# Kernel tuning notes

Hardware: AMD Instinct MI355X
Metric: run time of the kernel (lower is better)

## Reference

```python
import jax, jax.numpy as jnp
import numpy as np

EPS = 1e-5
C = 128
N, H, W = 16, 128, 128


def bn(x, g, b, m, v):
    # x: (N, C, H, W) or (N, C); params: (C,)
    sh = (1, -1) + (1,) * (x.ndim - 2)
    return (x - m.reshape(sh)) * (g.reshape(sh) / jnp.sqrt(v.reshape(sh) + EPS)) + b.reshape(sh)


def conv1x1(x, w, b=None):
    # x: (N, Cin, H, W), w: (Cout, Cin)
    y = jnp.einsum('oc,nchw->nohw', w, x)
    if b is not None:
        y = y + b.reshape(1, -1, 1, 1)
    return y


def setup_inputs() -> dict:
    key = jax.random.key(0)
    ks = jax.random.split(key, 20)
    C2 = C // 2
    Cr = C // 16
    d = {
        'f_vi': jax.random.normal(ks[0], (N, C, H, W), jnp.float32),
        'f_ir': jax.random.normal(ks[1], (N, C, H, W), jnp.float32),
        # channel_avg_attention: conv(2C->C/2)+BN+ReLU+conv(C/2->C)+BN+Sigmoid
        'ca1_w': jax.random.normal(ks[2], (C2, 2 * C), jnp.float32) * 0.05,
        'ca1_b': jnp.zeros((C2,), jnp.float32),
        'bn_a_g': jnp.ones((C2,), jnp.float32),
        'bn_a_b': jnp.zeros((C2,), jnp.float32),
        'bn_a_m': jnp.zeros((C2,), jnp.float32),
        'bn_a_v': jnp.ones((C2,), jnp.float32),
        'ca2_w': jax.random.normal(ks[3], (C, C2), jnp.float32) * 0.05,
        'ca2_b': jnp.zeros((C,), jnp.float32),
        'bn_b_g': jnp.ones((C,), jnp.float32),
        'bn_b_b': jnp.zeros((C,), jnp.float32),
        'bn_b_m': jnp.zeros((C,), jnp.float32),
        'bn_b_v': jnp.ones((C,), jnp.float32),
        # conv1: conv(2C->C)+BN+ReLU
        'conv1_w': jax.random.normal(ks[4], (C, 2 * C), jnp.float32) * 0.05,
        'conv1_b': jnp.zeros((C,), jnp.float32),
        'bn_c_g': jnp.ones((C,), jnp.float32),
        'bn_c_b': jnp.zeros((C,), jnp.float32),
        'bn_c_m': jnp.zeros((C,), jnp.float32),
        'bn_c_v': jnp.ones((C,), jnp.float32),
        # ChannelAttention shared MLP (no bias)
        'chatt_w1': jax.random.normal(ks[5], (Cr, C), jnp.float32) * 0.1,
        'chatt_w2': jax.random.normal(ks[6], (C, Cr), jnp.float32) * 0.1,
        # SpatialAttention 7x7 conv (no bias), (out=1, in=2, 7, 7)
        'sa_w': jax.random.normal(ks[7], (1, 2, 7, 7), jnp.float32) * 0.05,
    }
    return d


def reference(f_vi, f_ir, ca1_w, ca1_b, bn_a_g, bn_a_b, bn_a_m, bn_a_v,
              ca2_w, ca2_b, bn_b_g, bn_b_b, bn_b_m, bn_b_v,
              conv1_w, conv1_b, bn_c_g, bn_c_b, bn_c_m, bn_c_v,
              chatt_w1, chatt_w2, sa_w):
    c = f_vi.shape[1]
    f_cat = jnp.concatenate([f_vi, f_ir], axis=1)  # (N, 2C, H, W)

    # channel_avg_attention: GAP -> 1x1 conv -> BN -> ReLU -> 1x1 conv -> BN -> Sigmoid
    pooled = jnp.mean(f_cat, axis=(2, 3))  # (N, 2C)
    h = jax.nn.relu(bn(pooled @ ca1_w.T + ca1_b, bn_a_g, bn_a_b, bn_a_m, bn_a_v))
    wch = jax.nn.sigmoid(bn(h @ ca2_w.T + ca2_b, bn_b_g, bn_b_b, bn_b_m, bn_b_v))  # (N, C)
    w2 = jnp.concatenate([wch, wch], axis=1)[:, :, None, None]  # (N, 2C, 1, 1)

    f_cat = jnp.concatenate([f_ir, f_vi], axis=1) * w2 + f_cat  # complementary blend
    f_vi2, f_ir2 = f_cat[:, :c], f_cat[:, c:]

    g = jax.nn.relu(bn(conv1x1(f_cat, conv1_w, conv1_b), bn_c_g, bn_c_b, bn_c_m, bn_c_v))  # (N, C, H, W)

    # ChannelAttention on g
    avg = jnp.mean(g, axis=(2, 3))  # (N, C)
    mx = jnp.max(g, axis=(2, 3))    # (N, C)
    mlp = lambda x: jax.nn.relu(x @ chatt_w1.T) @ chatt_w2.T
    ca = jax.nn.sigmoid(mlp(avg) + mlp(mx))[:, :, None, None]  # (N, C, 1, 1)

    # SpatialAttention on g
    sp = jnp.stack([jnp.mean(g, axis=1), jnp.max(g, axis=1)], axis=1)  # (N, 2, H, W)
    sa = jax.lax.conv_general_dilated(sp, sa_w, window_strides=(1, 1), padding=[(3, 3), (3, 3)],
                                      dimension_numbers=('NCHW', 'OIHW', 'NCHW'))
    sa = jax.nn.sigmoid(sa)  # (N, 1, H, W)

    wgt = jax.nn.sigmoid(sa * ca)  # (N, C, H, W)
    return wgt * f_vi2 + (1.0 - wgt) * f_ir2
```

## Files before the change

### kernel.cpp

```cpp
#include <hip/hip_runtime.h>
#include <math.h>

#define CCH   128
#define C2    64
#define C2X   256
#define CR    8
#define HW    16384
#define NB    16
#define EPSB  1e-5f

#define WS_POOLED 0
#define WS_WCH    4096
#define WS_AVGS   6144
#define WS_MAXB   8192
#define WS_CA     10240
#define WS_BC     12288
#define WS_WV     16384
#define WS_WI     147456
#define WS_SPMEAN 278528
#define WS_SPMAX  540672
#define WS_SA     802816

typedef short short8 __attribute__((ext_vector_type(8)));
typedef float floatx4 __attribute__((ext_vector_type(4)));
typedef unsigned short ushort_t;
typedef unsigned int uint_t;

__device__ __forceinline__ float sigmoidf_(float x) {
    return 1.0f / (1.0f + __expf(-x));
}

__device__ __forceinline__ uint_t f2bf(float f) {
    uint_t u = __float_as_uint(f);
    return (u + 0x7FFFu + ((u >> 16) & 1u)) >> 16;
}
__device__ __forceinline__ uint_t pack2bf(float a, float b) {
    return f2bf(a) | (f2bf(b) << 16);
}

__global__ void k_pool(const float* __restrict__ fvi, const float* __restrict__ fir,
                       float* __restrict__ pooled) {
    int b  = blockIdx.x;
    int n  = b >> 8;
    int ch = b & 255;
    const float* src = (ch < CCH) ? (fvi + ((size_t)n * CCH + ch) * HW)
                                  : (fir + ((size_t)n * CCH + (ch - CCH)) * HW);
    const float4* s4 = (const float4*)src;
    float s0 = 0.f, s1 = 0.f, s2 = 0.f, s3 = 0.f;
    #pragma unroll
    for (int it = 0; it < 4; ++it) {
        float4 v0 = s4[threadIdx.x + (it * 4 + 0) * 256];
        float4 v1 = s4[threadIdx.x + (it * 4 + 1) * 256];
        float4 v2 = s4[threadIdx.x + (it * 4 + 2) * 256];
        float4 v3 = s4[threadIdx.x + (it * 4 + 3) * 256];
        s0 += (v0.x + v0.y) + (v0.z + v0.w);
        s1 += (v1.x + v1.y) + (v1.z + v1.w);
        s2 += (v2.x + v2.y) + (v2.z + v2.w);
        s3 += (v3.x + v3.y) + (v3.z + v3.w);
    }
    float sum = (s0 + s1) + (s2 + s3);
    #pragma unroll
    for (int off = 32; off > 0; off >>= 1) sum += __shfl_down(sum, off, 64);
    __shared__ float r[4];
    if ((threadIdx.x & 63) == 0) r[threadIdx.x >> 6] = sum;
    __syncthreads();
    if (threadIdx.x == 0)
        pooled[b] = (r[0] + r[1] + r[2] + r[3]) * (1.0f / HW);
}

__global__ void k_wch(const float* __restrict__ pooled,
                      const float* __restrict__ ca1_w, const float* __restrict__ ca1_b,
                      const float* __restrict__ ag, const float* __restrict__ ab,
                      const float* __restrict__ am, const float* __restrict__ av,
                      const float* __restrict__ ca2_w, const float* __restrict__ ca2_b,
                      const float* __restrict__ bg, const float* __restrict__ bb,
                      const float* __restrict__ bm, const float* __restrict__ bv,
                      float* __restrict__ wch) {
    int n = blockIdx.x;
    int t = threadIdx.x;
    __shared__ float h[C2];
    if (t < C2) {
        float acc = ca1_b[t];
        const float* w = ca1_w + t * C2X;
        const float* p = pooled + n * C2X;
        for (int k = 0; k < C2X; k++) acc += w[k] * p[k];
        float s = ag[t] * rsqrtf(av[t] + EPSB);
        acc = (acc - am[t]) * s + ab[t];
        h[t] = fmaxf(acc, 0.f);
    }
    __syncthreads();
    float acc = ca2_b[t];
    const float* w = ca2_w + t * C2;
    for (int j = 0; j < C2; j++) acc += w[j] * h[j];
    float s = bg[t] * rsqrtf(bv[t] + EPSB);
    acc = (acc - bm[t]) * s + bb[t];
    wch[n * CCH + t] = sigmoidf_(acc);
}

__global__ void k_mkweights(const float* __restrict__ wch, const float* __restrict__ conv1_w,
                            const float* __restrict__ cg, const float* __restrict__ cb,
                            const float* __restrict__ cm, const float* __restrict__ cv,
                            const float* __restrict__ conv1_b,
                            ushort_t* __restrict__ Wv, ushort_t* __restrict__ Wi,
                            float* __restrict__ Bc, float* __restrict__ zeroreg) {
    int b = blockIdx.x;
    int t = threadIdx.x;
    if (b < 16) { zeroreg[b * 256 + t] = 0.f; zeroreg[b * 256 + 128 + t] = 0.f; }
    if (b == 16) {
        float A = cg[t] * rsqrtf(cv[t] + EPSB);
        Bc[t] = A * (conv1_b[t] - cm[t]) + cb[t];
    }
    int n = b >> 7, o = b & 127;
    float A  = cg[o] * rsqrtf(cv[o] + EPSB);
    float u  = wch[n * CCH + t];
    float w0 = conv1_w[o * C2X + t];
    float w1 = conv1_w[o * C2X + t + CCH];
    Wv[(size_t)b * CCH + t] = (ushort_t)f2bf(A * (w0 + u * w1));
    Wi[(size_t)b * CCH + t] = (ushort_t)f2bf(A * (w1 + u * w0));
}

#define XR 64
__global__ __launch_bounds__(256)
void k_conv_reduce(const float* __restrict__ fvi, const float* __restrict__ fir,
                   const ushort_t* __restrict__ Wv, const ushort_t* __restrict__ Wi,
                   const float* __restrict__ Bc,
                   float* __restrict__ avgsum, uint_t* __restrict__ maxbits,
                   float* __restrict__ spmean, float* __restrict__ spmax) {
    int n  = blockIdx.x >> 7;
    int pt = blockIdx.x & 127;
    int p0 = pt * 128;

    __shared__ __align__(16) ushort_t sW[128 * XR];
    __shared__ __align__(16) ushort_t sX[128 * XR];

    int tid  = threadIdx.x;
    int wave = tid >> 6;
    int lane = tid & 63;
    int q    = lane >> 4;
    int ln   = lane & 15;

    floatx4 acc[2][8];
    #pragma unroll
    for (int a = 0; a < 2; a++)
        #pragma unroll
        for (int b = 0; b < 8; b++) acc[a][b] = (floatx4){0.f, 0.f, 0.f, 0.f};

    const float* pv = fvi + (size_t)n * CCH * HW + p0;
    const float* pi = fir + (size_t)n * CCH * HW + p0;
    const ushort_t* wvb = Wv + (size_t)n * CCH * CCH;
    const ushort_t* wib = Wi + (size_t)n * CCH * CCH;

    int wo  = tid >> 2, wc = tid & 3;
    int xpq = tid & 15, xcp = tid >> 4;
    int xch = xcp >> 2, xdw = xcp & 3;

    for (int ks = 0; ks < 8; ++ks) {
        const ushort_t* wsrc = (ks < 4) ? wvb : wib;
        const float*    xsrc = (ks < 4) ? pv  : pi;
        int c0 = (ks & 3) * 32;

        __syncthreads();
        #pragma unroll
        for (int it = 0; it < 2; ++it) {
            int o = it * 64 + wo;
            uint4 w4 = *(const uint4*)&wsrc[(size_t)o * CCH + c0 + wc * 8];
            *(uint4*)&sW[o * XR + ((wc ^ (o & 7)) << 3)] = w4;
        }
        #pragma unroll
        for (int it = 0; it < 2; ++it) {
            int pq = (it << 4) | xpq;
            const float* sp = xsrc + (size_t)(c0 + 2 * xcp) * HW + 4 * pq;
            float4 f1 = *(const float4*)sp;
            float4 f2 = *(const float4*)(sp + HW);
            int r0 = 4 * pq;
            *(uint_t*)&sX[(r0 + 0) * XR + ((xch ^ ((r0 + 0) & 7)) << 3) + xdw * 2] = pack2bf(f1.x, f2.x);
            *(uint_t*)&sX[(r0 + 1) * XR + ((xch ^ ((r0 + 1) & 7)) << 3) + xdw * 2] = pack2bf(f1.y, f2.y);
            *(uint_t*)&sX[(r0 + 2) * XR + ((xch ^ ((r0 + 2) & 7)) << 3) + xdw * 2] = pack2bf(f1.z, f2.z);
            *(uint_t*)&sX[(r0 + 3) * XR + ((xch ^ ((r0 + 3) & 7)) << 3) + xdw * 2] = pack2bf(f1.w, f2.w);
        }
        __syncthreads();

        short8 aW0, aW1;
        {
            int rA0 = wave * 32 + ln;
            int rA1 = rA0 + 16;
            aW0 = *(const short8*)&sW[rA0 * XR + ((q ^ (rA0 & 7)) << 3)];
            aW1 = *(const short8*)&sW[rA1 * XR + ((q ^ (rA1 & 7)) << 3)];
        }
        #pragma unroll
        for (int pj = 0; pj < 8; ++pj) {
            int rB = pj * 16 + ln;
            short8 bX = *(const short8*)&sX[rB * XR + ((q ^ (rB & 7)) << 3)];
            acc[0][pj] = __builtin_amdgcn_mfma_f32_16x16x32_bf16(aW0, bX, acc[0][pj], 0, 0, 0);
            acc[1][pj] = __builtin_amdgcn_mfma_f32_16x16x32_bf16(aW1, bX, acc[1][pj], 0, 0, 0);
        }
    }

    float bc[2][4];
    #pragma unroll
    for (int ot = 0; ot < 2; ++ot)
        #pragma unroll
        for (int r = 0; r < 4; ++r)
            bc[ot][r] = Bc[wave * 32 + ot * 16 + q * 4 + r];

    float rs[2][4], rm[2][4], ps[8], pm[8];
    #pragma unroll
    for (int ot = 0; ot < 2; ++ot)
        #pragma unroll
        for (int r = 0; r < 4; ++r) { rs[ot][r] = 0.f; rm[ot][r] = 0.f; }
    #pragma unroll
    for (int pj = 0; pj < 8; ++pj) { ps[pj] = 0.f; pm[pj] = 0.f; }

    #pragma unroll
    for (int ot = 0; ot < 2; ++ot)
        #pragma unroll
        for (int pj = 0; pj < 8; ++pj) {
            floatx4 a = acc[ot][pj];
            #pragma unroll
            for (int r = 0; r < 4; ++r) {
                float g = fmaxf(a[r] + bc[ot][r], 0.f);
                rs[ot][r] += g;
                rm[ot][r] = fmaxf(rm[ot][r], g);
                ps[pj] += g;
                pm[pj] = fmaxf(pm[pj], g);
            }
        }

    #pragma unroll
    for (int ot = 0; ot < 2; ++ot)
        #pragma unroll
        for (int r = 0; r < 4; ++r)
            #pragma unroll
            for (int off = 1; off < 16; off <<= 1) {
                rs[ot][r] += __shfl_xor(rs[ot][r], off, 64);
                rm[ot][r] = fmaxf(rm[ot][r], __shfl_xor(rm[ot][r], off, 64));
            }
    if (ln == 0) {
        #pragma unroll
        for (int ot = 0; ot < 2; ++ot)
            #pragma unroll
            for (int r = 0; r < 4; ++r) {
                int o = wave * 32 + ot * 16 + q * 4 + r;
                atomicAdd(&avgsum[n * CCH + o], rs[ot][r]);
                atomicMax(&maxbits[n * CCH + o], __float_as_uint(rm[ot][r]));
            }
    }

    #pragma unroll
    for (int pj = 0; pj < 8; ++pj) {
        #pragma unroll
        for (int off = 16; off < 64; off <<= 1) {
            ps[pj] += __shfl_xor(ps[pj], off, 64);
            pm[pj] = fmaxf(pm[pj], __shfl_xor(pm[pj], off, 64));
        }
    }
    __syncthreads();
    float* redS = (float*)sW;
    float* redM = (float*)sX;
    if (lane < 16) {
        #pragma unroll
        for (int pj = 0; pj < 8; ++pj) {
            redS[wave * 128 + pj * 16 + ln] = ps[pj];
            redM[wave * 128 + pj * 16 + ln] = pm[pj];
        }
    }
    __syncthreads();
    if (tid < 128) {
        float s = 0.f, m = 0.f;
        #pragma unroll
        for (int w = 0; w < 4; ++w) {
            s += redS[w * 128 + tid];
            m = fmaxf(m, redM[w * 128 + tid]);
        }
        spmean[(size_t)n * HW + p0 + tid] = s * (1.0f / CCH);
        spmax [(size_t)n * HW + p0 + tid] = m;
    }
}

__global__ void k_ca(const float* __restrict__ avgsum, const uint_t* __restrict__ maxbits,
                     const float* __restrict__ w1, const float* __restrict__ w2,
                     float* __restrict__ ca) {
    int n = blockIdx.x;
    int t = threadIdx.x;
    __shared__ float tsum[CR];
    if (t < CR) {
        float a = 0.f, m = 0.f;
        const float* w = w1 + t * CCH;
        for (int c = 0; c < CCH; c++) {
            a += w[c] * (avgsum[n * CCH + c] * (1.0f / HW));
            m += w[c] * __uint_as_float(maxbits[n * CCH + c]);
        }
        tsum[t] = fmaxf(a, 0.f) + fmaxf(m, 0.f);
    }
    __syncthreads();
    float s = 0.f;
    #pragma unroll
    for (int j = 0; j < CR; j++) s += w2[t * CR + j] * tsum[j];
    ca[n * CCH + t] = sigmoidf_(s);
}

__global__ void k_sa(const float* __restrict__ spmean, const float* __restrict__ spmax,
                     const float* __restrict__ sw, float* __restrict__ sa) {
    int b = blockIdx.x;
    int n = b >> 6;
    int y = ((b & 63) << 1) | (threadIdx.x >> 7);
    int x = threadIdx.x & 127;
    float acc = 0.f;
    for (int dy = -3; dy <= 3; dy++) {
        int yy = y + dy;
        if ((unsigned)yy >= 128u) continue;
        const float* rm = spmean + (size_t)n * HW + yy * 128;
        const float* rx = spmax  + (size_t)n * HW + yy * 128;
        #pragma unroll
        for (int dx = -3; dx <= 3; dx++) {
            int xx = x + dx;
            if ((unsigned)xx < 128u) {
                float wm = sw[(dy + 3) * 7 + (dx + 3)];
                float wx = sw[49 + (dy + 3) * 7 + (dx + 3)];
                acc += wm * rm[xx] + wx * rx[xx];
            }
        }
    }
    sa[(size_t)n * HW + y * 128 + x] = sigmoidf_(acc);
}

__global__ void k_out(const float4* __restrict__ fvi, const float4* __restrict__ fir,
                      const float* __restrict__ wch, const float* __restrict__ ca,
                      const float4* __restrict__ sa, float4* __restrict__ out) {
    size_t i0 = ((size_t)blockIdx.x * 256 + threadIdx.x) * 2;
    size_t i1 = i0 + 1;
    float4 a0 = fvi[i0], a1 = fvi[i1];
    float4 b0 = fir[i0], b1 = fir[i1];
    int p40 = (int)(i0 & 4095);
    int nc  = (int)(i0 >> 12);
    int n   = nc >> 7;
    float4 s0 = sa[(size_t)n * 4096 + p40];
    float4 s1 = sa[(size_t)n * 4096 + p40 + 1];
    float u  = wch[nc];
    float cv = ca[nc];
    float4 o0, o1;
    {
        float w = sigmoidf_(s0.x * cv);
        o0.x = w * (b0.x * u + a0.x) + (1.f - w) * (a0.x * u + b0.x);
    }
    {
        float w = sigmoidf_(s0.y * cv);
        o0.y = w * (b0.y * u + a0.y) + (1.f - w) * (a0.y * u + b0.y);
    }
    {
        float w = sigmoidf_(s0.z * cv);
        o0.z = w * (b0.z * u + a0.z) + (1.f - w) * (a0.z * u + b0.z);
    }
    {
        float w = sigmoidf_(s0.w * cv);
        o0.w = w * (b0.w * u + a0.w) + (1.f - w) * (a0.w * u + b0.w);
    }
    {
        float w = sigmoidf_(s1.x * cv);
        o1.x = w * (b1.x * u + a1.x) + (1.f - w) * (a1.x * u + b1.x);
    }
    {
        float w = sigmoidf_(s1.y * cv);
        o1.y = w * (b1.y * u + a1.y) + (1.f - w) * (a1.y * u + b1.y);
    }
    {
        float w = sigmoidf_(s1.z * cv);
        o1.z = w * (b1.z * u + a1.z) + (1.f - w) * (a1.z * u + b1.z);
    }
    {
        float w = sigmoidf_(s1.w * cv);
        o1.w = w * (b1.w * u + a1.w) + (1.f - w) * (a1.w * u + b1.w);
    }
    out[i0] = o0;
    out[i1] = o1;
}

extern "C" void kernel_launch(void* const* d_in, const int* in_sizes, int n_in,
                              void* d_out, int out_size, void* d_ws, size_t ws_size,
                              hipStream_t stream) {
    const float* fvi     = (const float*)d_in[0];
    const float* fir     = (const float*)d_in[1];
    const float* ca1_w   = (const float*)d_in[2];
    const float* ca1_b   = (const float*)d_in[3];
    const float* bn_a_g  = (const float*)d_in[4];
    const float* bn_a_b  = (const float*)d_in[5];
    const float* bn_a_m  = (const float*)d_in[6];
    const float* bn_a_v  = (const float*)d_in[7];
    const float* ca2_w   = (const float*)d_in[8];
    const float* ca2_b   = (const float*)d_in[9];
    const float* bn_b_g  = (const float*)d_in[10];
    const float* bn_b_b  = (const float*)d_in[11];
    const float* bn_b_m  = (const float*)d_in[12];
    const float* bn_b_v  = (const float*)d_in[13];
    const float* conv1_w = (const float*)d_in[14];
    const float* conv1_b = (const float*)d_in[15];
    const float* bn_c_g  = (const float*)d_in[16];
    const float* bn_c_b  = (const float*)d_in[17];
    const float* bn_c_m  = (const float*)d_in[18];
    const float* bn_c_v  = (const float*)d_in[19];
    const float* chatt_w1 = (const float*)d_in[20];
    const float* chatt_w2 = (const float*)d_in[21];
    const float* sa_w     = (const float*)d_in[22];

    float* ws = (float*)d_ws;
    float* out = (float*)d_out;

    k_pool<<<NB * C2X, 256, 0, stream>>>(fvi, fir, ws + WS_POOLED);
    k_wch<<<NB, 128, 0, stream>>>(ws + WS_POOLED, ca1_w, ca1_b,
                                  bn_a_g, bn_a_b, bn_a_m, bn_a_v,
                                  ca2_w, ca2_b, bn_b_g, bn_b_b, bn_b_m, bn_b_v,
                                  ws + WS_WCH);
    k_mkweights<<<NB * CCH, 128, 0, stream>>>(ws + WS_WCH, conv1_w,
                                              bn_c_g, bn_c_b, bn_c_m, bn_c_v, conv1_b,
                                              (ushort_t*)(ws + WS_WV), (ushort_t*)(ws + WS_WI),
                                              ws + WS_BC, ws + WS_AVGS);
    k_conv_reduce<<<NB * (HW / 128), 256, 0, stream>>>(fvi, fir,
                                                       (const ushort_t*)(ws + WS_WV),
                                                       (const ushort_t*)(ws + WS_WI),
                                                       ws + WS_BC,
                                                       ws + WS_AVGS, (uint_t*)(ws + WS_MAXB),
                                                       ws + WS_SPMEAN, ws + WS_SPMAX);
    k_ca<<<NB, 128, 0, stream>>>(ws + WS_AVGS, (const uint_t*)(ws + WS_MAXB),
                                 chatt_w1, chatt_w2, ws + WS_CA);
    k_sa<<<NB * 64, 256, 0, stream>>>(ws + WS_SPMEAN, ws + WS_SPMAX, sa_w, ws + WS_SA);
    k_out<<<(NB * CCH * HW / 4) / 512, 256, 0, stream>>>((const float4*)fvi, (const float4*)fir,
                                                         ws + WS_WCH, ws + WS_CA,
                                                         (const float4*)(ws + WS_SA), (float4*)out);
}
```

Before: 538.2 us.

## Fuse pooling with bf16 pre-packing and stream packed tiles into conv via LDS loads

The pooling kernel now also converts fvi/fir into swizzled bf16 tiles, written to the output buffer as scratch, and accumulates channel means with atomics after a separate zeroing kernel. The conv kernel keeps all weight fragments in registers and loads the packed tiles straight into LDS with global_load_lds, overlapping the second half of the load with MFMAs on the first. This replaces the fp32 re-read and per-iteration conversion and sync inside the conv with half-size bf16 reads. In exchange it adds an extra write and read of the bf16 blob, many atomics, and large LDS and register use. The output kernel's indexing is also changed to a coalesced stride.

```diff
diff --git a/kernel.cpp b/kernel.cpp
--- a/kernel.cpp
+++ b/kernel.cpp
@@ -26,6 +26,13 @@
 typedef unsigned short ushort_t;
 typedef unsigned int uint_t;
 
+#define GAS __attribute__((address_space(1)))
+#define LAS __attribute__((address_space(3)))
+
+__device__ __forceinline__ void gload16(const void* g, void* l) {
+    __builtin_amdgcn_global_load_lds((const GAS void*)g, (LAS void*)l, 16, 0, 0);
+}
+
 __device__ __forceinline__ float sigmoidf_(float x) {
     return 1.0f / (1.0f + __expf(-x));
 }
@@ -38,34 +45,53 @@
     return f2bf(a) | (f2bf(b) << 16);
 }
 
-__global__ void k_pool(const float* __restrict__ fvi, const float* __restrict__ fir,
-                       float* __restrict__ pooled) {
+__global__ void k_zero(float* __restrict__ p) {
+    p[blockIdx.x * 256 + threadIdx.x] = 0.f;
+}
+
+__global__ __launch_bounds__(256)
+void k_prep(const float* __restrict__ fvi, const float* __restrict__ fir,
+            ushort_t* __restrict__ blob, float* __restrict__ pooled) {
     int b  = blockIdx.x;
+    int st = b & 1;
+    int pt = (b >> 1) & 127;
     int n  = b >> 8;
-    int ch = b & 255;
-    const float* src = (ch < CCH) ? (fvi + ((size_t)n * CCH + ch) * HW)
-                                  : (fir + ((size_t)n * CCH + (ch - CCH)) * HW);
-    const float4* s4 = (const float4*)src;
-    float s0 = 0.f, s1 = 0.f, s2 = 0.f, s3 = 0.f;
-    #pragma unroll
-    for (int it = 0; it < 4; ++it) {
-        float4 v0 = s4[threadIdx.x + (it * 4 + 0) * 256];
-        float4 v1 = s4[threadIdx.x + (it * 4 + 1) * 256];
-        float4 v2 = s4[threadIdx.x + (it * 4 + 2) * 256];
-        float4 v3 = s4[threadIdx.x + (it * 4 + 3) * 256];
-        s0 += (v0.x + v0.y) + (v0.z + v0.w);
-        s1 += (v1.x + v1.y) + (v1.z + v1.w);
-        s2 += (v2.x + v2.y) + (v2.z + v2.w);
-        s3 += (v3.x + v3.y) + (v3.z + v3.w);
-    }
-    float sum = (s0 + s1) + (s2 + s3);
-    #pragma unroll
-    for (int off = 32; off > 0; off >>= 1) sum += __shfl_down(sum, off, 64);
-    __shared__ float r[4];
-    if ((threadIdx.x & 63) == 0) r[threadIdx.x >> 6] = sum;
+    const float* src = (st == 0 ? fvi : fir) + (size_t)n * CCH * HW + pt * 128;
+    __shared__ __align__(16) ushort_t img[128 * 128];
+    int t = threadIdx.x;
+    int p = t & 127;
+    int cg = t >> 7;
+    const float inv = 1.0f / HW;
+    #pragma unroll
+    for (int i = 0; i < 8; ++i) {
+        int cidx = cg * 8 + i;
+        const float* sc = src + (size_t)(cidx * 8) * HW + p;
+        float v0 = sc[0];        float v1 = sc[HW];
+        float v2 = sc[2 * HW];   float v3 = sc[3 * HW];
+        float v4 = sc[4 * HW];   float v5 = sc[5 * HW];
+        float v6 = sc[6 * HW];   float v7 = sc[7 * HW];
+        uint4 pk;
+        pk.x = pack2bf(v0, v1);  pk.y = pack2bf(v2, v3);
+        pk.z = pack2bf(v4, v5);  pk.w = pack2bf(v6, v7);
+        *(uint4*)&img[p * 128 + ((cidx ^ (p & 7)) << 3)] = pk;
+        float ss[8] = {v0, v1, v2, v3, v4, v5, v6, v7};
+        #pragma unroll
+        for (int j = 0; j < 8; ++j) {
+            float s = ss[j] * inv;
+            #pragma unroll
+            for (int off = 1; off < 64; off <<= 1)
+                s += __shfl_xor(s, off, 64);
+            if ((t & 63) == 0)
+                atomicAdd(&pooled[n * 256 + st * 128 + cidx * 8 + j], s);
+        }
+    }
     __syncthreads();
-    if (threadIdx.x == 0)
-        pooled[b] = (r[0] + r[1] + r[2] + r[3]) * (1.0f / HW);
+    ushort_t* dst = blob + (size_t)b * 16384;
+    #pragma unroll
+    for (int j = 0; j < 8; ++j) {
+        int off = (j * 256 + t) * 8;
+        *(uint4*)&dst[off] = *(const uint4*)&img[off];
+    }
 }
 
 __global__ void k_wch(const float* __restrict__ pooled,
@@ -119,9 +145,8 @@
     Wi[(size_t)b * CCH + t] = (ushort_t)f2bf(A * (w1 + u * w0));
 }
 
-#define XR 64
 __global__ __launch_bounds__(256)
-void k_conv_reduce(const float* __restrict__ fvi, const float* __restrict__ fir,
+void k_conv_reduce(const ushort_t* __restrict__ blob,
                    const ushort_t* __restrict__ Wv, const ushort_t* __restrict__ Wi,
                    const float* __restrict__ Bc,
                    float* __restrict__ avgsum, uint_t* __restrict__ maxbits,
@@ -129,70 +154,69 @@
     int n  = blockIdx.x >> 7;
     int pt = blockIdx.x & 127;
     int p0 = pt * 128;
-
-    __shared__ __align__(16) ushort_t sW[128 * XR];
-    __shared__ __align__(16) ushort_t sX[128 * XR];
-
+    __shared__ __align__(16) ushort_t sX[32768];
     int tid  = threadIdx.x;
     int wave = tid >> 6;
     int lane = tid & 63;
     int q    = lane >> 4;
     int ln   = lane & 15;
 
+    short8 aF[2][8];
+    {
+        const ushort_t* wv = Wv + (size_t)n * 16384;
+        const ushort_t* wi = Wi + (size_t)n * 16384;
+        #pragma unroll
+        for (int kc = 0; kc < 8; ++kc) {
+            const ushort_t* ws_ = (kc < 4) ? wv : wi;
+            #pragma unroll
+            for (int ot = 0; ot < 2; ++ot) {
+                int o = wave * 32 + ot * 16 + ln;
+                aF[ot][kc] = *(const short8*)&ws_[(size_t)o * 128 + (kc & 3) * 32 + q * 8];
+            }
+        }
+    }
+    __builtin_amdgcn_sched_barrier(0);
+    {
+        const ushort_t* gb = blob + (((size_t)(n * 128 + pt)) << 15) + wave * 512 + lane * 8;
+        ushort_t* lb = &sX[wave * 512];
+        #pragma unroll
+        for (int i = 0; i < 16; ++i)
+            gload16(gb + i * 2048, lb + i * 2048);
+    }
+    __builtin_amdgcn_sched_barrier(0);
+
     floatx4 acc[2][8];
     #pragma unroll
     for (int a = 0; a < 2; a++)
         #pragma unroll
-        for (int b = 0; b < 8; b++) acc[a][b] = (floatx4){0.f, 0.f, 0.f, 0.f};
-
-    const float* pv = fvi + (size_t)n * CCH * HW + p0;
-    const float* pi = fir + (size_t)n * CCH * HW + p0;
-    const ushort_t* wvb = Wv + (size_t)n * CCH * CCH;
-    const ushort_t* wib = Wi + (size_t)n * CCH * CCH;
-
-    int wo  = tid >> 2, wc = tid & 3;
-    int xpq = tid & 15, xcp = tid >> 4;
-    int xch = xcp >> 2, xdw = xcp & 3;
-
-    for (int ks = 0; ks < 8; ++ks) {
-        const ushort_t* wsrc = (ks < 4) ? wvb : wib;
-        const float*    xsrc = (ks < 4) ? pv  : pi;
-        int c0 = (ks & 3) * 32;
-
-        __syncthreads();
-        #pragma unroll
-        for (int it = 0; it < 2; ++it) {
-            int o = it * 64 + wo;
-            uint4 w4 = *(const uint4*)&wsrc[(size_t)o * CCH + c0 + wc * 8];
-            *(uint4*)&sW[o * XR + ((wc ^ (o & 7)) << 3)] = w4;
-        }
-        #pragma unroll
-        for (int it = 0; it < 2; ++it) {
-            int pq = (it << 4) | xpq;
-            const float* sp = xsrc + (size_t)(c0 + 2 * xcp) * HW + 4 * pq;
-            float4 f1 = *(const float4*)sp;
-            float4 f2 = *(const float4*)(sp + HW);
-            int r0 = 4 * pq;
-            *(uint_t*)&sX[(r0 + 0) * XR + ((xch ^ ((r0 + 0) & 7)) << 3) + xdw * 2] = pack2bf(f1.x, f2.x);
-            *(uint_t*)&sX[(r0 + 1) * XR + ((xch ^ ((r0 + 1) & 7)) << 3) + xdw * 2] = pack2bf(f1.y, f2.y);
-            *(uint_t*)&sX[(r0 + 2) * XR + ((xch ^ ((r0 + 2) & 7)) << 3) + xdw * 2] = pack2bf(f1.z, f2.z);
-            *(uint_t*)&sX[(r0 + 3) * XR + ((xch ^ ((r0 + 3) & 7)) << 3) + xdw * 2] = pack2bf(f1.w, f2.w);
-        }
-        __syncthreads();
-
-        short8 aW0, aW1;
-        {
-            int rA0 = wave * 32 + ln;
-            int rA1 = rA0 + 16;
-            aW0 = *(const short8*)&sW[rA0 * XR + ((q ^ (rA0 & 7)) << 3)];
-            aW1 = *(const short8*)&sW[rA1 * XR + ((q ^ (rA1 & 7)) << 3)];
-        }
+        for (int c = 0; c < 8; c++) acc[a][c] = (floatx4){0.f, 0.f, 0.f, 0.f};
+
+    asm volatile("s_waitcnt vmcnt(8)" ::: "memory");
+    __builtin_amdgcn_s_barrier();
+    __builtin_amdgcn_sched_barrier(0);
+    #pragma unroll
+    for (int kc = 0; kc < 4; ++kc) {
         #pragma unroll
         for (int pj = 0; pj < 8; ++pj) {
-            int rB = pj * 16 + ln;
-            short8 bX = *(const short8*)&sX[rB * XR + ((q ^ (rB & 7)) << 3)];
-            acc[0][pj] = __builtin_amdgcn_mfma_f32_16x16x32_bf16(aW0, bX, acc[0][pj], 0, 0, 0);
-            acc[1][pj] = __builtin_amdgcn_mfma_f32_16x16x32_bf16(aW1, bX, acc[1][pj], 0, 0, 0);
+            int p = pj * 16 + ln;
+            int cidx = kc * 4 + q;
+            short8 bX = *(const short8*)&sX[p * 128 + ((cidx ^ (p & 7)) << 3)];
+            acc[0][pj] = __builtin_amdgcn_mfma_f32_16x16x32_bf16(aF[0][kc], bX, acc[0][pj], 0, 0, 0);
+            acc[1][pj] = __builtin_amdgcn_mfma_f32_16x16x32_bf16(aF[1][kc], bX, acc[1][pj], 0, 0, 0);
+        }
+    }
+    asm volatile("s_waitcnt vmcnt(0)" ::: "memory");
+    __builtin_amdgcn_s_barrier();
+    __builtin_amdgcn_sched_barrier(0);
+    #pragma unroll
+    for (int kc = 4; kc < 8; ++kc) {
+        #pragma unroll
+        for (int pj = 0; pj < 8; ++pj) {
+            int p = pj * 16 + ln;
+            int cidx = (kc & 3) * 4 + q;
+            short8 bX = *(const short8*)&sX[16384 + p * 128 + ((cidx ^ (p & 7)) << 3)];
+            acc[0][pj] = __builtin_amdgcn_mfma_f32_16x16x32_bf16(aF[0][kc], bX, acc[0][pj], 0, 0, 0);
+            acc[1][pj] = __builtin_amdgcn_mfma_f32_16x16x32_bf16(aF[1][kc], bX, acc[1][pj], 0, 0, 0);
         }
     }
 
@@ -255,8 +279,8 @@
         }
     }
     __syncthreads();
-    float* redS = (float*)sW;
-    float* redM = (float*)sX;
+    float* redS = (float*)sX;
+    float* redM = redS + 512;
     if (lane < 16) {
         #pragma unroll
         for (int pj = 0; pj < 8; ++pj) {
@@ -327,15 +351,15 @@
 __global__ void k_out(const float4* __restrict__ fvi, const float4* __restrict__ fir,
                       const float* __restrict__ wch, const float* __restrict__ ca,
                       const float4* __restrict__ sa, float4* __restrict__ out) {
-    size_t i0 = ((size_t)blockIdx.x * 256 + threadIdx.x) * 2;
-    size_t i1 = i0 + 1;
+    size_t i0 = (size_t)blockIdx.x * 512 + threadIdx.x;
+    size_t i1 = i0 + 256;
+    int nc  = (int)(i0 >> 12);
+    int n   = nc >> 7;
+    int p40 = (int)(i0 & 4095);
     float4 a0 = fvi[i0], a1 = fvi[i1];
     float4 b0 = fir[i0], b1 = fir[i1];
-    int p40 = (int)(i0 & 4095);
-    int nc  = (int)(i0 >> 12);
-    int n   = nc >> 7;
     float4 s0 = sa[(size_t)n * 4096 + p40];
-    float4 s1 = sa[(size_t)n * 4096 + p40 + 1];
+    float4 s1 = sa[(size_t)n * 4096 + p40 + 256];
     float u  = wch[nc];
     float cv = ca[nc];
     float4 o0, o1;
@@ -402,10 +426,12 @@
     const float* chatt_w2 = (const float*)d_in[21];
     const float* sa_w     = (const float*)d_in[22];
 
-    float* ws = (float*)d_ws;
+    float* ws  = (float*)d_ws;
     float* out = (float*)d_out;
-
-    k_pool<<<NB * C2X, 256, 0, stream>>>(fvi, fir, ws + WS_POOLED);
+    ushort_t* blob = (ushort_t*)d_out;
+
+    k_zero<<<16, 256, 0, stream>>>(ws + WS_POOLED);
+    k_prep<<<NB * 128 * 2, 256, 0, stream>>>(fvi, fir, blob, ws + WS_POOLED);
     k_wch<<<NB, 128, 0, stream>>>(ws + WS_POOLED, ca1_w, ca1_b,
                                   bn_a_g, bn_a_b, bn_a_m, bn_a_v,
                                   ca2_w, ca2_b, bn_b_g, bn_b_b, bn_b_m, bn_b_v,
@@ -414,7 +440,7 @@
                                               bn_c_g, bn_c_b, bn_c_m, bn_c_v, conv1_b,
                                               (ushort_t*)(ws + WS_WV), (ushort_t*)(ws + WS_WI),
                                               ws + WS_BC, ws + WS_AVGS);
-    k_conv_reduce<<<NB * (HW / 128), 256, 0, stream>>>(fvi, fir,
+    k_conv_reduce<<<NB * (HW / 128), 256, 0, stream>>>(blob,
                                                        (const ushort_t*)(ws + WS_WV),
                                                        (const ushort_t*)(ws + WS_WI),
                                                        ws + WS_BC,
```

Measured after the change: 824.0 us. 53.1% more time.
